# Kernel tuning notes

Hardware: AMD Instinct MI355X
Metric: run time of the kernel (lower is better)

Reference implementation:

```python
import jax, jax.numpy as jnp
import numpy as np

B, D, N, OUT, H = 32768, 256, 4, 512, 4
DH = D // H


def _layer_norm(x, g, b, eps=1e-5):
    mu = jnp.mean(x, axis=-1, keepdims=True)
    var = jnp.mean(jnp.square(x - mu), axis=-1, keepdims=True)
    return (x - mu) * jax.lax.rsqrt(var + eps) * g + b


def setup_inputs() -> dict:
    key = jax.random.key(0)
    ks = jax.random.split(key, 32)
    s = lambda i, shape, scale=0.02: (jax.random.normal(ks[i], shape, jnp.float32) * scale)
    inp = {
        'w0': jax.random.normal(ks[0], (B, D), jnp.float32),
        'w1': jax.random.normal(ks[1], (B, D), jnp.float32),
        'w2': jax.random.normal(ks[2], (B, D), jnp.float32),
        'w3': jax.random.normal(ks[3], (B, D), jnp.float32),
        'regime': jax.random.uniform(ks[4], (B, 4), jnp.float32),
        'tf_weights': jnp.array([0.5, 1.0, 1.5, 2.0], jnp.float32),
        'in_proj_w': s(5, (3 * D, D)),
        'in_proj_b': s(6, (3 * D,)),
        'out_proj_w': s(7, (D, D)),
        'out_proj_b': s(8, (D,)),
        'ln1_g': jnp.ones((D,), jnp.float32),
        'ln1_b': jnp.zeros((D,), jnp.float32),
        'sg_w': s(9, (D, 4)),
        'sg_b': s(10, (D,)),
        'sb_w': s(11, (D, 4)),
        'sb_b': s(12, (D,)),
        'f1_w': s(13, (2 * OUT, D * N)),
        'f1_b': s(14, (2 * OUT,)),
        'f2_w': s(15, (OUT, 2 * OUT)),
        'f2_b': s(16, (OUT,)),
        'ln2_g': jnp.ones((OUT,), jnp.float32),
        'ln2_b': jnp.zeros((OUT,), jnp.float32),
        'a1_w': s(17, (128, D * N)),
        'a1_b': s(18, (128,)),
        'a2_w': s(19, (1, 128)),
        'a2_b': s(20, (1,)),
    }
    return inp


def _forward(w0, w1, w2, w3, regime, tf_weights, in_proj_w, in_proj_b,
             out_proj_w, out_proj_b, ln1_g, ln1_b, sg_w, sg_b, sb_w, sb_b,
             f1_w, f1_b, f2_w, f2_b, ln2_g, ln2_b, a1_w, a1_b, a2_w, a2_b):
    weights = jax.nn.softmax(tf_weights)  # [N]
    wav = jnp.stack([w0, w1, w2, w3], axis=1)  # [B, N, D]
    weighted = wav * weights[None, :, None]    # [B, N, D]
    query = weighted[:, 0, :]                  # [B, D]

    # MultiheadAttention: q_len=1, kv_len=N, H heads
    wq, wk, wv = in_proj_w[:D], in_proj_w[D:2 * D], in_proj_w[2 * D:]
    bq, bk, bv = in_proj_b[:D], in_proj_b[D:2 * D], in_proj_b[2 * D:]
    q = (query @ wq.T + bq).reshape(B, H, DH)              # [B, H, Dh]
    k = (weighted @ wk.T + bk).reshape(B, N, H, DH)        # [B, N, H, Dh]
    v = (weighted @ wv.T + bv).reshape(B, N, H, DH)
    scores = jnp.einsum('bhd,bnhd->bhn', q, k) / jnp.sqrt(jnp.float32(DH))
    attn = jax.nn.softmax(scores, axis=-1)                 # [B, H, N]
    ctx = jnp.einsum('bhn,bnhd->bhd', attn, v).reshape(B, D)
    attn_out = ctx @ out_proj_w.T + out_proj_b             # [B, D]

    entry = _layer_norm(query + attn_out, ln1_g, ln1_b)    # [B, D]
    gamma = regime @ sg_w.T + sg_b
    beta = regime @ sb_w.T + sb_b
    entry = entry * (1.0 + gamma) + beta                   # FiLM

    cat = jnp.concatenate([entry, weighted[:, 1, :], weighted[:, 2, :], weighted[:, 3, :]], axis=-1)  # [B, D*N]
    h = jax.nn.gelu(cat @ f1_w.T + f1_b, approximate=False)
    fused = _layer_norm(h @ f2_w.T + f2_b, ln2_g, ln2_b)   # [B, OUT]

    a = jax.nn.gelu(cat @ a1_w.T + a1_b, approximate=False)
    alignment = jax.nn.sigmoid(a @ a2_w.T + a2_b)          # [B, 1]
    return fused, alignment


def reference(w0, w1, w2, w3, regime, tf_weights, in_proj_w, in_proj_b,
              out_proj_w, out_proj_b, ln1_g, ln1_b, sg_w, sg_b, sb_w, sb_b,
              f1_w, f1_b, f2_w, f2_b, ln2_g, ln2_b, a1_w, a1_b, a2_w, a2_b):
    return _forward(w0, w1, w2, w3, regime, tf_weights, in_proj_w, in_proj_b,
                    out_proj_w, out_proj_b, ln1_g, ln1_b, sg_w, sg_b, sb_w, sb_b,
                    f1_w, f1_b, f2_w, f2_b, ln2_g, ln2_b, a1_w, a1_b, a2_w, a2_b)
```

## Files before the change

kernel.cpp:

```cpp
#include <hip/hip_runtime.h>
#include <math.h>

#define NB 32768

typedef unsigned short u16;
typedef __attribute__((ext_vector_type(4))) float f32x4;
typedef __attribute__((ext_vector_type(8))) short bf16x8;

__device__ __forceinline__ float bf2f(u16 u){ return __uint_as_float(((unsigned int)u)<<16); }
__device__ __forceinline__ u16 f2bf(float f){
    unsigned int x = __float_as_uint(f);
    x += 0x7fffu + ((x>>16)&1u);
    return (u16)(x>>16);
}
__device__ __forceinline__ float gelu_f(float x){
    float z = fabsf(x) * 0.70710678118654752f;
    float t = __builtin_amdgcn_rcpf(1.0f + 0.3275911f*z);
    float p = t*(0.254829592f + t*(-0.284496736f + t*(1.421413741f + t*(-1.453152027f + t*1.061405429f))));
    float e = __expf(-z*z);
    float erf_abs = 1.0f - p*e;
    float erfv = copysignf(erf_abs, x);
    return 0.5f*x*(1.0f + erfv);
}

__device__ __forceinline__ void gload16(const void* g, void* l){
    __builtin_amdgcn_global_load_lds(
        (const __attribute__((address_space(1))) unsigned int*)g,
        (__attribute__((address_space(3))) unsigned int*)l, 16, 0, 0);
}

__global__ __launch_bounds__(256) void prepconv_kernel(
    const float* __restrict__ w0, const float* __restrict__ w1,
    const float* __restrict__ w2, const float* __restrict__ w3,
    const float* __restrict__ tfw, u16* __restrict__ wcat,
    const float* __restrict__ ipw_s, u16* __restrict__ ipw_d,
    const float* __restrict__ op_s,  u16* __restrict__ op_d,
    const float* __restrict__ f1_s,  u16* __restrict__ f1_d,
    const float* __restrict__ f2_s,  u16* __restrict__ f2_d,
    const float* __restrict__ a1_s,  u16* __restrict__ a1_d)
{
    const int blk = blockIdx.x, tid = threadIdx.x;
    if (blk < 8192){
        float t0=tfw[0], t1=tfw[1], t2=tfw[2], t3=tfw[3];
        float m = fmaxf(fmaxf(t0,t1), fmaxf(t2,t3));
        float e0=expf(t0-m), e1=expf(t1-m), e2=expf(t2-m), e3=expf(t3-m);
        float inv = 1.0f/(e0+e1+e2+e3);
        float s0=e0*inv, s1=e1*inv, s2=e2*inv, s3=e3*inv;

        int idx = blk*256 + tid;
        int b  = idx >> 6;
        int d4 = (idx & 63) << 2;
        size_t src = (size_t)b*256 + d4;
        float4 a0 = *reinterpret_cast<const float4*>(w0 + src);
        float4 a1 = *reinterpret_cast<const float4*>(w1 + src);
        float4 a2 = *reinterpret_cast<const float4*>(w2 + src);
        float4 a3 = *reinterpret_cast<const float4*>(w3 + src);
        size_t dst = (size_t)b*1024 + d4;
        ushort4 o;
        o.x=f2bf(a0.x*s0); o.y=f2bf(a0.y*s0); o.z=f2bf(a0.z*s0); o.w=f2bf(a0.w*s0);
        *reinterpret_cast<ushort4*>(wcat + dst) = o;
        o.x=f2bf(a1.x*s1); o.y=f2bf(a1.y*s1); o.z=f2bf(a1.z*s1); o.w=f2bf(a1.w*s1);
        *reinterpret_cast<ushort4*>(wcat + dst + 256) = o;
        o.x=f2bf(a2.x*s2); o.y=f2bf(a2.y*s2); o.z=f2bf(a2.z*s2); o.w=f2bf(a2.w*s2);
        *reinterpret_cast<ushort4*>(wcat + dst + 512) = o;
        o.x=f2bf(a3.x*s3); o.y=f2bf(a3.y*s3); o.z=f2bf(a3.z*s3); o.w=f2bf(a3.w*s3);
        *reinterpret_cast<ushort4*>(wcat + dst + 768) = o;
    } else {
        int i = (blk - 8192)*256 + tid;
        const float* s; u16* d; int off;
        if      (i < 49152)  { s=ipw_s; d=ipw_d; off=i; }
        else if (i < 65536)  { s=op_s;  d=op_d;  off=i-49152; }
        else if (i < 327680) { s=f1_s;  d=f1_d;  off=i-65536; }
        else if (i < 458752) { s=f2_s;  d=f2_d;  off=i-327680; }
        else                 { s=a1_s;  d=a1_d;  off=i-458752; }
        float4 v = reinterpret_cast<const float4*>(s)[off];
        ushort4 o; o.x=f2bf(v.x); o.y=f2bf(v.y); o.z=f2bf(v.z); o.w=f2bf(v.w);
        reinterpret_cast<ushort4*>(d)[off] = o;
    }
}

template<int ACT>
__global__ __launch_bounds__(256) void mgemm_kernel(
    const u16* __restrict__ A, int lda,
    const u16* __restrict__ W, int ldw,
    const float* __restrict__ bias,
    u16* __restrict__ C, int ldc, int K,
    const float* __restrict__ a2w, const float* __restrict__ a2b, float* __restrict__ aln)
{
    __shared__ __align__(16) u16 sA[4096];
    __shared__ __align__(16) u16 sB[4096];

    const int tid  = threadIdx.x;
    const int lane = tid & 63;
    const int wid  = tid >> 6;
    const int wr   = wid >> 1, wc = wid & 1;
    const int row0 = blockIdx.x << 7, col0 = blockIdx.y << 7;

    const int e0 = tid << 3,          r0s = e0 >> 5, c0s = e0 & 31;
    const int e1 = (256 + tid) << 3,  r1s = e1 >> 5, c1s = e1 & 31;
    const u16* gA0 = A + (size_t)(row0 + r0s)*lda + c0s;
    const u16* gA1 = A + (size_t)(row0 + r1s)*lda + c1s;
    const u16* gB0 = W + (size_t)(col0 + r0s)*ldw + c0s;
    const u16* gB1 = W + (size_t)(col0 + r1s)*ldw + c1s;
    u16* lA0 = sA + (wid << 9);
    u16* lA1 = sA + 2048 + (wid << 9);
    u16* lB0 = sB + (wid << 9);
    u16* lB1 = sB + 2048 + (wid << 9);

    const int la  = lane & 15;
    const int lk  = (lane >> 4) << 3;
    const int hi4 = (lane >> 4) << 2;
    const u16* rA = sA + (((wr << 6) + la) << 5) + lk;
    const u16* rB = sB + (((wc << 6) + la) << 5) + lk;

    f32x4 acc[4][4];
    {
        f32x4 binit[4];
        #pragma unroll
        for (int n=0;n<4;n++){
            float4 b4 = *reinterpret_cast<const float4*>(bias + col0 + (wc<<6) + (n<<4) + hi4);
            binit[n] = (f32x4){b4.x, b4.y, b4.z, b4.w};
        }
        #pragma unroll
        for (int m=0;m<4;m++)
            #pragma unroll
            for (int n=0;n<4;n++) acc[m][n] = binit[n];
    }

    for (int k0 = 0; k0 < K; k0 += 32){
        gload16(gA0 + k0, lA0);
        gload16(gA1 + k0, lA1);
        gload16(gB0 + k0, lB0);
        gload16(gB1 + k0, lB1);
        __syncthreads();
        bf16x8 af[4], bf[4];
        #pragma unroll
        for (int m=0;m<4;m++) af[m] = *reinterpret_cast<const bf16x8*>(rA + (m << 9));
        #pragma unroll
        for (int n=0;n<4;n++) bf[n] = *reinterpret_cast<const bf16x8*>(rB + (n << 9));
        #pragma unroll
        for (int m=0;m<4;m++)
            #pragma unroll
            for (int n=0;n<4;n++)
                acc[m][n] = __builtin_amdgcn_mfma_f32_16x16x32_bf16(bf[n], af[m], acc[m][n], 0, 0, 0);
        __syncthreads();
    }

    if (ACT == 2){
        float w4[4][4];
        #pragma unroll
        for (int n=0;n<4;n++){
            float4 t4 = *reinterpret_cast<const float4*>(a2w + (wc<<6) + (n<<4) + hi4);
            w4[n][0]=t4.x; w4[n][1]=t4.y; w4[n][2]=t4.z; w4[n][3]=t4.w;
        }
        float* red = reinterpret_cast<float*>(sA);
        #pragma unroll
        for (int m=0;m<4;m++){
            float p = 0.f;
            #pragma unroll
            for (int n=0;n<4;n++){
                f32x4 v = acc[m][n];
                p += gelu_f(v[0])*w4[n][0] + gelu_f(v[1])*w4[n][1]
                   + gelu_f(v[2])*w4[n][2] + gelu_f(v[3])*w4[n][3];
            }
            red[(((wr<<6) + (m<<4) + la) << 3) + (wc<<2) + (lane>>4)] = p;
        }
        __syncthreads();
        if (tid < 128){
            float s = 0.f;
            #pragma unroll
            for (int k2=0;k2<8;k2++) s += red[(tid<<3)+k2];
            aln[row0 + tid] = 1.0f/(1.0f + __expf(-(s + a2b[0])));
        }
        return;
    }

    #pragma unroll
    for (int m=0;m<4;m++){
        const int grow = row0 + (wr << 6) + (m << 4) + la;
        u16* crow = C + (size_t)grow*ldc + col0 + (wc << 6) + hi4;
        #pragma unroll
        for (int n=0;n<4;n++){
            f32x4 v = acc[m][n];
            float x0=v[0], x1=v[1], x2=v[2], x3=v[3];
            if (ACT == 1){ x0=gelu_f(x0); x1=gelu_f(x1); x2=gelu_f(x2); x3=gelu_f(x3); }
            ushort4 o; o.x=f2bf(x0); o.y=f2bf(x1); o.z=f2bf(x2); o.w=f2bf(x3);
            *reinterpret_cast<ushort4*>(crow + (n << 4)) = o;
        }
    }
}

template<int ACT>
__global__ __launch_bounds__(512) void gemm256p_kernel(
    const u16* __restrict__ A, int lda,
    const u16* __restrict__ W, int ldw,
    const float* __restrict__ bias,
    u16* __restrict__ C, int ldc, int K)
{
    __shared__ __align__(16) u16 sT[65536];

    const int tid  = threadIdx.x;
    const int lane = tid & 63;
    const int wid  = tid >> 6;
    const int wr   = wid >> 2;
    const int wc   = wid & 3;
    const int row0 = blockIdx.x << 8, col0 = blockIdx.y << 8;

    const int la = lane & 15;
    const int hi = lane >> 4;

    f32x4 acc[8][4];
    {
        f32x4 binit[4];
        #pragma unroll
        for (int n=0;n<4;n++){
            float4 b4 = *reinterpret_cast<const float4*>(bias + col0 + (wc<<6) + (n<<4) + (hi<<2));
            binit[n] = (f32x4){b4.x, b4.y, b4.z, b4.w};
        }
        #pragma unroll
        for (int m=0;m<8;m++)
            #pragma unroll
            for (int n=0;n<4;n++) acc[m][n] = binit[n];
    }

    const int rs = (wid << 4) + (lane >> 3);
    const int cs = ((lane & 7) ^ ((lane >> 3) & 7)) << 3;
    const u16* gA0 = A + (size_t)(row0 + rs)*lda + cs;
    const u16* gA1 = gA0 + (size_t)128*lda;
    const u16* gB0 = W + (size_t)(col0 + rs)*ldw + cs;
    const u16* gB1 = gB0 + (size_t)128*ldw;
    const int ldsw = (wid << 4) * 64;

    const int cph0 = (hi ^ (la & 7)) << 3;
    const u16* rAbase = sT + ((wr << 7) + la)*64;
    const u16* rBbase = sT + 16384 + ((wc << 6) + la)*64;

    const int NT = K >> 6;

    gload16(gB0, sT + 16384 + ldsw);          gload16(gB0 + 8*(size_t)ldw, sT + 16384 + ldsw + 512);
    gload16(gB1, sT + 24576 + ldsw);          gload16(gB1 + 8*(size_t)ldw, sT + 24576 + ldsw + 512);
    gload16(gA0, sT + ldsw);                  gload16(gA0 + 8*(size_t)lda, sT + ldsw + 512);
    gload16(gA1, sT + 8192 + ldsw);           gload16(gA1 + 8*(size_t)lda, sT + 8192 + ldsw + 512);

#define STG(GP, LD, DOFF) \
        gload16(GP + kb, sT + bn + (DOFF) + ldsw); \
        gload16(GP + kb + 8*(size_t)(LD), sT + bn + (DOFF) + ldsw + 512);

#define DSR(MH, KS) { \
        const int co_ = cph0 ^ ((KS) << 5); \
        const u16* rA_ = rAbase + b + ((MH) << 12) + co_; \
        const u16* rB_ = rBbase + b + co_; \
        af[0] = *reinterpret_cast<const bf16x8*>(rA_); \
        af[1] = *reinterpret_cast<const bf16x8*>(rA_ + 1024); \
        af[2] = *reinterpret_cast<const bf16x8*>(rA_ + 2048); \
        af[3] = *reinterpret_cast<const bf16x8*>(rA_ + 3072); \
        bf[0] = *reinterpret_cast<const bf16x8*>(rB_); \
        bf[1] = *reinterpret_cast<const bf16x8*>(rB_ + 1024); \
        bf[2] = *reinterpret_cast<const bf16x8*>(rB_ + 2048); \
        bf[3] = *reinterpret_cast<const bf16x8*>(rB_ + 3072); }

#define MFMA16(MB) { \
        __builtin_amdgcn_s_setprio(1); \
        _Pragma("unroll") \
        for (int m=0;m<4;m++){ \
            _Pragma("unroll") \
            for (int n=0;n<4;n++) \
                acc[(MB)+m][n] = __builtin_amdgcn_mfma_f32_16x16x32_bf16(bf[n], af[m], acc[(MB)+m][n], 0,0,0); \
        } \
        __builtin_amdgcn_s_setprio(0); }

    for (int t = 0; t < NT; ++t){
        const int b  = (t & 1) << 15;
        const int bn = b ^ 32768;
        const bool stg = (t + 1 < NT);
        const int kb = (t + 1) << 6;
        bf16x8 af[4], bf[4];

        asm volatile("s_waitcnt vmcnt(0)" ::: "memory");
        __builtin_amdgcn_s_barrier();
        __builtin_amdgcn_sched_barrier(0);
        DSR(0,0)
        if (stg){ STG(gB0, ldw, 16384) }
        MFMA16(0)
        DSR(1,0)
        if (stg){ STG(gB1, ldw, 24576) }
        __builtin_amdgcn_sched_barrier(0);
        __builtin_amdgcn_s_barrier();
        __builtin_amdgcn_sched_barrier(0);
        MFMA16(4)
        DSR(0,1)
        if (stg){ STG(gA0, lda, 0) }
        __builtin_amdgcn_sched_barrier(0);
        __builtin_amdgcn_s_barrier();
        __builtin_amdgcn_sched_barrier(0);
        MFMA16(0)
        DSR(1,1)
        if (stg){ STG(gA1, lda, 8192) }
        __builtin_amdgcn_sched_barrier(0);
        __builtin_amdgcn_s_barrier();
        __builtin_amdgcn_sched_barrier(0);
        MFMA16(4)
    }
#undef STG
#undef DSR
#undef MFMA16

    #pragma unroll
    for (int m=0;m<8;m++){
        const int grow = row0 + (wr << 7) + (m << 4) + la;
        u16* crow = C + (size_t)grow*ldc + col0 + (wc << 6) + (hi << 2);
        #pragma unroll
        for (int n=0;n<4;n++){
            f32x4 v = acc[m][n];
            float x0=v[0], x1=v[1], x2=v[2], x3=v[3];
            if (ACT == 1){ x0=gelu_f(x0); x1=gelu_f(x1); x2=gelu_f(x2); x3=gelu_f(x3); }
            ushort4 o; o.x=f2bf(x0); o.y=f2bf(x1); o.z=f2bf(x2); o.w=f2bf(x3);
            *reinterpret_cast<ushort4*>(crow + (n << 4)) = o;
        }
    }
}

__global__ __launch_bounds__(256) void attn_kernel(
    const u16* __restrict__ q, const u16* __restrict__ kv,
    u16* __restrict__ ctx)
{
    __shared__ float sQ[256], sK[1024], sV[1024], sS[16], sA[16];
    const int b = blockIdx.x, t = threadIdx.x;
    sQ[t] = bf2f(q[(size_t)b*256 + t]);
    #pragma unroll
    for (int n=0;n<4;n++){
        sK[n*256+t] = bf2f(kv[(size_t)b*2048 + n*512 + t]);
        sV[n*256+t] = bf2f(kv[(size_t)b*2048 + n*512 + 256 + t]);
    }
    __syncthreads();
    if (t < 16){
        int h = t>>2, n = t&3;
        float s = 0.f;
        const int o = h*64;
        #pragma unroll
        for (int dh=0; dh<64; ++dh) s += sQ[o+dh]*sK[n*256+o+dh];
        sS[t] = s * 0.125f;
    }
    __syncthreads();
    if (t < 4){
        float a0=sS[t*4+0], a1=sS[t*4+1], a2=sS[t*4+2], a3=sS[t*4+3];
        float m = fmaxf(fmaxf(a0,a1), fmaxf(a2,a3));
        float e0=expf(a0-m), e1=expf(a1-m), e2=expf(a2-m), e3=expf(a3-m);
        float inv = 1.0f/(e0+e1+e2+e3);
        sA[t*4+0]=e0*inv; sA[t*4+1]=e1*inv; sA[t*4+2]=e2*inv; sA[t*4+3]=e3*inv;
    }
    __syncthreads();
    const int h = t>>6;
    float c = sA[h*4+0]*sV[t] + sA[h*4+1]*sV[256+t] + sA[h*4+2]*sV[512+t] + sA[h*4+3]*sV[768+t];
    ctx[(size_t)b*256 + t] = f2bf(c);
}

__global__ __launch_bounds__(256) void lnfilm_kernel(
    u16* __restrict__ wcat, const u16* __restrict__ ao, const float* __restrict__ regime,
    const float* __restrict__ sgw, const float* __restrict__ sgb,
    const float* __restrict__ sbw, const float* __restrict__ sbb,
    const float* __restrict__ g1, const float* __restrict__ b1)
{
    const int b = blockIdx.x, t = threadIdx.x;
    float x = bf2f(wcat[(size_t)b*1024 + t]) + bf2f(ao[(size_t)b*256 + t]);
    float s = x, q = x*x;
    #pragma unroll
    for (int o=32;o;o>>=1){ s += __shfl_xor(s,o); q += __shfl_xor(q,o); }
    __shared__ float rs[4], rq[4];
    if ((t&63)==0){ rs[t>>6]=s; rq[t>>6]=q; }
    __syncthreads();
    s = rs[0]+rs[1]+rs[2]+rs[3];
    q = rq[0]+rq[1]+rq[2]+rq[3];
    float mu  = s*(1.0f/256.0f);
    float var = q*(1.0f/256.0f) - mu*mu;
    float rstd = rsqrtf(var + 1e-5f);
    float r0=regime[b*4+0], r1=regime[b*4+1], r2=regime[b*4+2], r3=regime[b*4+3];
    float gam = r0*sgw[t*4+0]+r1*sgw[t*4+1]+r2*sgw[t*4+2]+r3*sgw[t*4+3]+sgb[t];
    float bet = r0*sbw[t*4+0]+r1*sbw[t*4+1]+r2*sbw[t*4+2]+r3*sbw[t*4+3]+sbb[t];
    float e = ((x-mu)*rstd*g1[t]+b1[t])*(1.0f+gam)+bet;
    wcat[(size_t)b*1024 + t] = f2bf(e);
}

__global__ __launch_bounds__(256) void ln2_kernel(
    const u16* __restrict__ t1, const float* __restrict__ g, const float* __restrict__ bt,
    float* __restrict__ out)
{
    const int b = blockIdx.x, t = threadIdx.x;
    float x0 = bf2f(t1[(size_t)b*512 + t]);
    float x1 = bf2f(t1[(size_t)b*512 + 256 + t]);
    float s = x0+x1, q = x0*x0 + x1*x1;
    #pragma unroll
    for (int o=32;o;o>>=1){ s += __shfl_xor(s,o); q += __shfl_xor(q,o); }
    __shared__ float rs[4], rq[4];
    if ((t&63)==0){ rs[t>>6]=s; rq[t>>6]=q; }
    __syncthreads();
    s = rs[0]+rs[1]+rs[2]+rs[3];
    q = rq[0]+rq[1]+rq[2]+rq[3];
    float mu  = s*(1.0f/512.0f);
    float var = q*(1.0f/512.0f) - mu*mu;
    float rstd = rsqrtf(var + 1e-5f);
    out[(size_t)b*512 + t]       = (x0-mu)*rstd*g[t]     + bt[t];
    out[(size_t)b*512 + 256 + t] = (x1-mu)*rstd*g[256+t] + bt[256+t];
}

extern "C" void kernel_launch(void* const* d_in, const int* in_sizes, int n_in,
                              void* d_out, int out_size, void* d_ws, size_t ws_size,
                              hipStream_t stream) {
    const float* w0   = (const float*)d_in[0];
    const float* w1   = (const float*)d_in[1];
    const float* w2   = (const float*)d_in[2];
    const float* w3   = (const float*)d_in[3];
    const float* regime = (const float*)d_in[4];
    const float* tfw  = (const float*)d_in[5];
    const float* in_proj_w = (const float*)d_in[6];
    const float* in_proj_b = (const float*)d_in[7];
    const float* out_proj_w = (const float*)d_in[8];
    const float* out_proj_b = (const float*)d_in[9];
    const float* ln1_g = (const float*)d_in[10];
    const float* ln1_b = (const float*)d_in[11];
    const float* sg_w = (const float*)d_in[12];
    const float* sg_b = (const float*)d_in[13];
    const float* sb_w = (const float*)d_in[14];
    const float* sb_b = (const float*)d_in[15];
    const float* f1_w = (const float*)d_in[16];
    const float* f1_b = (const float*)d_in[17];
    const float* f2_w = (const float*)d_in[18];
    const float* f2_b = (const float*)d_in[19];
    const float* ln2_g = (const float*)d_in[20];
    const float* ln2_b = (const float*)d_in[21];
    const float* a1_w = (const float*)d_in[22];
    const float* a1_b = (const float*)d_in[23];
    const float* a2_w = (const float*)d_in[24];
    const float* a2_b = (const float*)d_in[25];

    char* ws = (char*)d_ws;
    u16* wcat  = (u16*)(ws);
    u16* qbuf  = (u16*)(ws + 67108864ull);
    u16* kvbuf = (u16*)(ws + 83886080ull);
    u16* hbuf  = kvbuf;
    u16* t1buf = (u16*)(ws + 150994944ull);
    u16* aobuf = (u16*)(ws + 184549376ull);
    u16* wb    = (u16*)(ws + 218103808ull);
    u16* ipw = wb;
    u16* opw = wb + 196608;
    u16* f1w = wb + 262144;
    u16* f2w = wb + 1310720;
    u16* a1w = wb + 1835008;

    float* out_fused = (float*)d_out;
    float* out_align = (float*)d_out + (size_t)NB*512;

    prepconv_kernel<<<10112, 256, 0, stream>>>(w0,w1,w2,w3,tfw,wcat,
        in_proj_w,ipw, out_proj_w,opw, f1_w,f1w, f2_w,f2w, a1_w,a1w);
    mgemm_kernel<0><<<dim3(256, 2), 256, 0, stream>>>(wcat, 1024, ipw, 256, in_proj_b, qbuf, 256, 256, nullptr, nullptr, nullptr);
    gemm256p_kernel<0><<<dim3(512, 2), 512, 0, stream>>>(wcat, 256, ipw+65536, 256, in_proj_b+256, kvbuf, 512, 256);
    attn_kernel<<<NB, 256, 0, stream>>>(qbuf, kvbuf, qbuf);
    mgemm_kernel<0><<<dim3(256, 2), 256, 0, stream>>>(qbuf, 256, opw, 256, out_proj_b, aobuf, 256, 256, nullptr, nullptr, nullptr);
    lnfilm_kernel<<<NB, 256, 0, stream>>>(wcat, aobuf, regime, sg_w, sg_b, sb_w, sb_b, ln1_g, ln1_b);
    gemm256p_kernel<1><<<dim3(128, 4), 512, 0, stream>>>(wcat, 1024, f1w, 1024, f1_b, hbuf, 1024, 1024);
    gemm256p_kernel<0><<<dim3(128, 2), 512, 0, stream>>>(hbuf, 1024, f2w, 1024, f2_b, t1buf, 512, 1024);
    ln2_kernel<<<NB, 256, 0, stream>>>(t1buf, ln2_g, ln2_b, out_fused);
    mgemm_kernel<2><<<dim3(256, 1), 256, 0, stream>>>(wcat, 1024, a1w, 1024, a1_b, qbuf, 128, 1024, a2_w, a2_b, out_align);
}
```

Before: 357.0 us.

## Shrink GEMM K-tile to 32 with single-barrier double-buffered pipeline

```diff
diff --git a/kernel.cpp b/kernel.cpp
--- a/kernel.cpp
+++ b/kernel.cpp
@@ -191,13 +191,13 @@
 }
 
 template<int ACT>
-__global__ __launch_bounds__(512) void gemm256p_kernel(
+__global__ __launch_bounds__(512) void gemm256b_kernel(
     const u16* __restrict__ A, int lda,
     const u16* __restrict__ W, int ldw,
     const float* __restrict__ bias,
     u16* __restrict__ C, int ldc, int K)
 {
-    __shared__ __align__(16) u16 sT[65536];
+    __shared__ __align__(16) u16 sT[32768];
 
     const int tid  = threadIdx.x;
     const int lane = tid & 63;
@@ -208,13 +208,14 @@
 
     const int la = lane & 15;
     const int hi = lane >> 4;
+    const int hi4 = hi << 2;
 
     f32x4 acc[8][4];
     {
         f32x4 binit[4];
         #pragma unroll
         for (int n=0;n<4;n++){
-            float4 b4 = *reinterpret_cast<const float4*>(bias + col0 + (wc<<6) + (n<<4) + (hi<<2));
+            float4 b4 = *reinterpret_cast<const float4*>(bias + col0 + (wc<<6) + (n<<4) + hi4);
             binit[n] = (f32x4){b4.x, b4.y, b4.z, b4.w};
         }
         #pragma unroll
@@ -223,92 +224,93 @@
             for (int n=0;n<4;n++) acc[m][n] = binit[n];
     }
 
-    const int rs = (wid << 4) + (lane >> 3);
-    const int cs = ((lane & 7) ^ ((lane >> 3) & 7)) << 3;
-    const u16* gA0 = A + (size_t)(row0 + rs)*lda + cs;
-    const u16* gA1 = gA0 + (size_t)128*lda;
-    const u16* gB0 = W + (size_t)(col0 + rs)*ldw + cs;
-    const u16* gB1 = gB0 + (size_t)128*ldw;
-    const int ldsw = (wid << 4) * 64;
-
-    const int cph0 = (hi ^ (la & 7)) << 3;
-    const u16* rAbase = sT + ((wr << 7) + la)*64;
-    const u16* rBbase = sT + 16384 + ((wc << 6) + la)*64;
-
-    const int NT = K >> 6;
-
-    gload16(gB0, sT + 16384 + ldsw);          gload16(gB0 + 8*(size_t)ldw, sT + 16384 + ldsw + 512);
-    gload16(gB1, sT + 24576 + ldsw);          gload16(gB1 + 8*(size_t)ldw, sT + 24576 + ldsw + 512);
-    gload16(gA0, sT + ldsw);                  gload16(gA0 + 8*(size_t)lda, sT + ldsw + 512);
-    gload16(gA1, sT + 8192 + ldsw);           gload16(gA1 + 8*(size_t)lda, sT + 8192 + ldsw + 512);
-
-#define STG(GP, LD, DOFF) \
-        gload16(GP + kb, sT + bn + (DOFF) + ldsw); \
-        gload16(GP + kb + 8*(size_t)(LD), sT + bn + (DOFF) + ldsw + 512);
-
-#define DSR(MH, KS) { \
-        const int co_ = cph0 ^ ((KS) << 5); \
-        const u16* rA_ = rAbase + b + ((MH) << 12) + co_; \
-        const u16* rB_ = rBbase + b + co_; \
-        af[0] = *reinterpret_cast<const bf16x8*>(rA_); \
-        af[1] = *reinterpret_cast<const bf16x8*>(rA_ + 1024); \
-        af[2] = *reinterpret_cast<const bf16x8*>(rA_ + 2048); \
-        af[3] = *reinterpret_cast<const bf16x8*>(rA_ + 3072); \
-        bf[0] = *reinterpret_cast<const bf16x8*>(rB_); \
-        bf[1] = *reinterpret_cast<const bf16x8*>(rB_ + 1024); \
-        bf[2] = *reinterpret_cast<const bf16x8*>(rB_ + 2048); \
-        bf[3] = *reinterpret_cast<const bf16x8*>(rB_ + 3072); }
-
-#define MFMA16(MB) { \
-        __builtin_amdgcn_s_setprio(1); \
-        _Pragma("unroll") \
-        for (int m=0;m<4;m++){ \
-            _Pragma("unroll") \
-            for (int n=0;n<4;n++) \
-                acc[(MB)+m][n] = __builtin_amdgcn_mfma_f32_16x16x32_bf16(bf[n], af[m], acc[(MB)+m][n], 0,0,0); \
-        } \
-        __builtin_amdgcn_s_setprio(0); }
+    const int rA0 = (wid << 5) + (lane >> 2);
+    const int rA1 = rA0 + 16;
+    const int sw0 = ((lane & 3) ^ ((rA0 >> 1) & 3)) << 3;
+    const int sw1 = ((lane & 3) ^ ((rA1 >> 1) & 3)) << 3;
+    const u16* pA0 = A + (size_t)(row0 + rA0)*lda + sw0;
+    const u16* pA1 = A + (size_t)(row0 + rA1)*lda + sw1;
+    const u16* pB0 = W + (size_t)(col0 + rA0)*ldw + sw0;
+    const u16* pB1 = W + (size_t)(col0 + rA1)*ldw + sw1;
+    const int ldsw = wid << 10;
+
+    const int cph0 = (hi ^ ((la >> 1) & 3)) << 3;
+    const u16* rAbase = sT + (((wr << 7) + la) << 5) + cph0;
+    const u16* rBbase = sT + 8192 + (((wc << 6) + la) << 5) + cph0;
+
+    const int NT = K >> 5;
+
+    gload16(pB0, sT + 8192 + ldsw);   gload16(pB1, sT + 8192 + ldsw + 512);
+    gload16(pA0, sT + ldsw);          gload16(pA1, sT + ldsw + 512);
 
     for (int t = 0; t < NT; ++t){
-        const int b  = (t & 1) << 15;
-        const int bn = b ^ 32768;
-        const bool stg = (t + 1 < NT);
-        const int kb = (t + 1) << 6;
-        bf16x8 af[4], bf[4];
+        const int b  = (t & 1) << 14;
+        const int bn = b ^ 16384;
+        const int kb = (t + 1) << 5;
 
         asm volatile("s_waitcnt vmcnt(0)" ::: "memory");
         __builtin_amdgcn_s_barrier();
-        __builtin_amdgcn_sched_barrier(0);
-        DSR(0,0)
-        if (stg){ STG(gB0, ldw, 16384) }
-        MFMA16(0)
-        DSR(1,0)
-        if (stg){ STG(gB1, ldw, 24576) }
-        __builtin_amdgcn_sched_barrier(0);
-        __builtin_amdgcn_s_barrier();
-        __builtin_amdgcn_sched_barrier(0);
-        MFMA16(4)
-        DSR(0,1)
-        if (stg){ STG(gA0, lda, 0) }
-        __builtin_amdgcn_sched_barrier(0);
-        __builtin_amdgcn_s_barrier();
-        __builtin_amdgcn_sched_barrier(0);
-        MFMA16(0)
-        DSR(1,1)
-        if (stg){ STG(gA1, lda, 8192) }
-        __builtin_amdgcn_sched_barrier(0);
-        __builtin_amdgcn_s_barrier();
-        __builtin_amdgcn_sched_barrier(0);
-        MFMA16(4)
-    }
-#undef STG
-#undef DSR
-#undef MFMA16
+
+        if (t + 1 < NT){
+            gload16(pB0 + kb, sT + bn + 8192 + ldsw);   gload16(pB1 + kb, sT + bn + 8192 + ldsw + 512);
+            gload16(pA0 + kb, sT + bn + ldsw);          gload16(pA1 + kb, sT + bn + ldsw + 512);
+        }
+
+        const u16* rA = rAbase + b;
+        const u16* rB = rBbase + b;
+        bf16x8 af0 = *reinterpret_cast<const bf16x8*>(rA);
+        bf16x8 af1 = *reinterpret_cast<const bf16x8*>(rA + 512);
+        bf16x8 af2 = *reinterpret_cast<const bf16x8*>(rA + 1024);
+        bf16x8 af3 = *reinterpret_cast<const bf16x8*>(rA + 1536);
+        bf16x8 bf0 = *reinterpret_cast<const bf16x8*>(rB);
+        bf16x8 bf1 = *reinterpret_cast<const bf16x8*>(rB + 512);
+        bf16x8 bf2 = *reinterpret_cast<const bf16x8*>(rB + 1024);
+        bf16x8 bf3 = *reinterpret_cast<const bf16x8*>(rB + 1536);
+        bf16x8 af4 = *reinterpret_cast<const bf16x8*>(rA + 2048);
+        bf16x8 af5 = *reinterpret_cast<const bf16x8*>(rA + 2560);
+        bf16x8 af6 = *reinterpret_cast<const bf16x8*>(rA + 3072);
+        bf16x8 af7 = *reinterpret_cast<const bf16x8*>(rA + 3584);
+
+        __builtin_amdgcn_s_setprio(1);
+        acc[0][0] = __builtin_amdgcn_mfma_f32_16x16x32_bf16(bf0, af0, acc[0][0], 0,0,0);
+        acc[0][1] = __builtin_amdgcn_mfma_f32_16x16x32_bf16(bf1, af0, acc[0][1], 0,0,0);
+        acc[0][2] = __builtin_amdgcn_mfma_f32_16x16x32_bf16(bf2, af0, acc[0][2], 0,0,0);
+        acc[0][3] = __builtin_amdgcn_mfma_f32_16x16x32_bf16(bf3, af0, acc[0][3], 0,0,0);
+        acc[1][0] = __builtin_amdgcn_mfma_f32_16x16x32_bf16(bf0, af1, acc[1][0], 0,0,0);
+        acc[1][1] = __builtin_amdgcn_mfma_f32_16x16x32_bf16(bf1, af1, acc[1][1], 0,0,0);
+        acc[1][2] = __builtin_amdgcn_mfma_f32_16x16x32_bf16(bf2, af1, acc[1][2], 0,0,0);
+        acc[1][3] = __builtin_amdgcn_mfma_f32_16x16x32_bf16(bf3, af1, acc[1][3], 0,0,0);
+        acc[2][0] = __builtin_amdgcn_mfma_f32_16x16x32_bf16(bf0, af2, acc[2][0], 0,0,0);
+        acc[2][1] = __builtin_amdgcn_mfma_f32_16x16x32_bf16(bf1, af2, acc[2][1], 0,0,0);
+        acc[2][2] = __builtin_amdgcn_mfma_f32_16x16x32_bf16(bf2, af2, acc[2][2], 0,0,0);
+        acc[2][3] = __builtin_amdgcn_mfma_f32_16x16x32_bf16(bf3, af2, acc[2][3], 0,0,0);
+        acc[3][0] = __builtin_amdgcn_mfma_f32_16x16x32_bf16(bf0, af3, acc[3][0], 0,0,0);
+        acc[3][1] = __builtin_amdgcn_mfma_f32_16x16x32_bf16(bf1, af3, acc[3][1], 0,0,0);
+        acc[3][2] = __builtin_amdgcn_mfma_f32_16x16x32_bf16(bf2, af3, acc[3][2], 0,0,0);
+        acc[3][3] = __builtin_amdgcn_mfma_f32_16x16x32_bf16(bf3, af3, acc[3][3], 0,0,0);
+        acc[4][0] = __builtin_amdgcn_mfma_f32_16x16x32_bf16(bf0, af4, acc[4][0], 0,0,0);
+        acc[4][1] = __builtin_amdgcn_mfma_f32_16x16x32_bf16(bf1, af4, acc[4][1], 0,0,0);
+        acc[4][2] = __builtin_amdgcn_mfma_f32_16x16x32_bf16(bf2, af4, acc[4][2], 0,0,0);
+        acc[4][3] = __builtin_amdgcn_mfma_f32_16x16x32_bf16(bf3, af4, acc[4][3], 0,0,0);
+        acc[5][0] = __builtin_amdgcn_mfma_f32_16x16x32_bf16(bf0, af5, acc[5][0], 0,0,0);
+        acc[5][1] = __builtin_amdgcn_mfma_f32_16x16x32_bf16(bf1, af5, acc[5][1], 0,0,0);
+        acc[5][2] = __builtin_amdgcn_mfma_f32_16x16x32_bf16(bf2, af5, acc[5][2], 0,0,0);
+        acc[5][3] = __builtin_amdgcn_mfma_f32_16x16x32_bf16(bf3, af5, acc[5][3], 0,0,0);
+        acc[6][0] = __builtin_amdgcn_mfma_f32_16x16x32_bf16(bf0, af6, acc[6][0], 0,0,0);
+        acc[6][1] = __builtin_amdgcn_mfma_f32_16x16x32_bf16(bf1, af6, acc[6][1], 0,0,0);
+        acc[6][2] = __builtin_amdgcn_mfma_f32_16x16x32_bf16(bf2, af6, acc[6][2], 0,0,0);
+        acc[6][3] = __builtin_amdgcn_mfma_f32_16x16x32_bf16(bf3, af6, acc[6][3], 0,0,0);
+        acc[7][0] = __builtin_amdgcn_mfma_f32_16x16x32_bf16(bf0, af7, acc[7][0], 0,0,0);
+        acc[7][1] = __builtin_amdgcn_mfma_f32_16x16x32_bf16(bf1, af7, acc[7][1], 0,0,0);
+        acc[7][2] = __builtin_amdgcn_mfma_f32_16x16x32_bf16(bf2, af7, acc[7][2], 0,0,0);
+        acc[7][3] = __builtin_amdgcn_mfma_f32_16x16x32_bf16(bf3, af7, acc[7][3], 0,0,0);
+        __builtin_amdgcn_s_setprio(0);
+    }
 
     #pragma unroll
     for (int m=0;m<8;m++){
         const int grow = row0 + (wr << 7) + (m << 4) + la;
-        u16* crow = C + (size_t)grow*ldc + col0 + (wc << 6) + (hi << 2);
+        u16* crow = C + (size_t)grow*ldc + col0 + (wc << 6) + hi4;
         #pragma unroll
         for (int n=0;n<4;n++){
             f32x4 v = acc[m][n];
@@ -453,12 +455,12 @@
     prepconv_kernel<<<10112, 256, 0, stream>>>(w0,w1,w2,w3,tfw,wcat,
         in_proj_w,ipw, out_proj_w,opw, f1_w,f1w, f2_w,f2w, a1_w,a1w);
     mgemm_kernel<0><<<dim3(256, 2), 256, 0, stream>>>(wcat, 1024, ipw, 256, in_proj_b, qbuf, 256, 256, nullptr, nullptr, nullptr);
-    gemm256p_kernel<0><<<dim3(512, 2), 512, 0, stream>>>(wcat, 256, ipw+65536, 256, in_proj_b+256, kvbuf, 512, 256);
+    gemm256b_kernel<0><<<dim3(512, 2), 512, 0, stream>>>(wcat, 256, ipw+65536, 256, in_proj_b+256, kvbuf, 512, 256);
     attn_kernel<<<NB, 256, 0, stream>>>(qbuf, kvbuf, qbuf);
     mgemm_kernel<0><<<dim3(256, 2), 256, 0, stream>>>(qbuf, 256, opw, 256, out_proj_b, aobuf, 256, 256, nullptr, nullptr, nullptr);
     lnfilm_kernel<<<NB, 256, 0, stream>>>(wcat, aobuf, regime, sg_w, sg_b, sb_w, sb_b, ln1_g, ln1_b);
-    gemm256p_kernel<1><<<dim3(128, 4), 512, 0, stream>>>(wcat, 1024, f1w, 1024, f1_b, hbuf, 1024, 1024);
-    gemm256p_kernel<0><<<dim3(128, 2), 512, 0, stream>>>(hbuf, 1024, f2w, 1024, f2_b, t1buf, 512, 1024);
+    gemm256b_kernel<1><<<dim3(128, 4), 512, 0, stream>>>(wcat, 1024, f1w, 1024, f1_b, hbuf, 1024, 1024);
+    gemm256b_kernel<0><<<dim3(128, 2), 512, 0, stream>>>(hbuf, 1024, f2w, 1024, f2_b, t1buf, 512, 1024);
     ln2_kernel<<<NB, 256, 0, stream>>>(t1buf, ln2_g, ln2_b, out_fused);
     mgemm_kernel<2><<<dim3(256, 1), 256, 0, stream>>>(wcat, 1024, a1w, 1024, a1_b, qbuf, 128, 1024, a2_w, a2_b, out_align);
 }
```

Result: slower. 368.5 us (+3.2%).

## Switch 256x256 GEMM to 32x32x16 MFMA and simplify staging schedule

Applied to the files above, without the earlier changes.

```diff
diff --git a/kernel.cpp b/kernel.cpp
--- a/kernel.cpp
+++ b/kernel.cpp
@@ -4,8 +4,9 @@
 #define NB 32768
 
 typedef unsigned short u16;
-typedef __attribute__((ext_vector_type(4))) float f32x4;
-typedef __attribute__((ext_vector_type(8))) short bf16x8;
+typedef __attribute__((ext_vector_type(4)))  float f32x4;
+typedef __attribute__((ext_vector_type(16))) float f32x16;
+typedef __attribute__((ext_vector_type(8)))  short bf16x8;
 
 __device__ __forceinline__ float bf2f(u16 u){ return __uint_as_float(((unsigned int)u)<<16); }
 __device__ __forceinline__ u16 f2bf(float f){
@@ -191,7 +192,7 @@
 }
 
 template<int ACT>
-__global__ __launch_bounds__(512) void gemm256p_kernel(
+__global__ __launch_bounds__(512) void gemm256c_kernel(
     const u16* __restrict__ A, int lda,
     const u16* __restrict__ W, int ldw,
     const float* __restrict__ bias,
@@ -206,21 +207,20 @@
     const int wc   = wid & 3;
     const int row0 = blockIdx.x << 8, col0 = blockIdx.y << 8;
 
-    const int la = lane & 15;
-    const int hi = lane >> 4;
-
-    f32x4 acc[8][4];
-    {
-        f32x4 binit[4];
-        #pragma unroll
-        for (int n=0;n<4;n++){
-            float4 b4 = *reinterpret_cast<const float4*>(bias + col0 + (wc<<6) + (n<<4) + (hi<<2));
-            binit[n] = (f32x4){b4.x, b4.y, b4.z, b4.w};
-        }
-        #pragma unroll
-        for (int m=0;m<8;m++)
-            #pragma unroll
-            for (int n=0;n<4;n++) acc[m][n] = binit[n];
+    const int l31 = lane & 31;
+    const int hi5 = lane >> 5;
+
+    f32x16 acc[4][2];
+    #pragma unroll
+    for (int nf=0; nf<2; nf++){
+        f32x16 bi;
+        #pragma unroll
+        for (int q=0; q<4; q++){
+            float4 b4 = *reinterpret_cast<const float4*>(bias + col0 + (wc<<6) + (nf<<5) + (q<<3) + (hi5<<2));
+            bi[4*q+0]=b4.x; bi[4*q+1]=b4.y; bi[4*q+2]=b4.z; bi[4*q+3]=b4.w;
+        }
+        #pragma unroll
+        for (int mf=0; mf<4; mf++) acc[mf][nf] = bi;
     }
 
     const int rs = (wid << 4) + (lane >> 3);
@@ -231,91 +231,69 @@
     const u16* gB1 = gB0 + (size_t)128*ldw;
     const int ldsw = (wid << 4) * 64;
 
-    const int cph0 = (hi ^ (la & 7)) << 3;
-    const u16* rAbase = sT + ((wr << 7) + la)*64;
-    const u16* rBbase = sT + 16384 + ((wc << 6) + la)*64;
+    const int arow = (wr << 7) + l31;
+    const int brow = (wc << 6) + l31;
 
     const int NT = K >> 6;
 
-    gload16(gB0, sT + 16384 + ldsw);          gload16(gB0 + 8*(size_t)ldw, sT + 16384 + ldsw + 512);
-    gload16(gB1, sT + 24576 + ldsw);          gload16(gB1 + 8*(size_t)ldw, sT + 24576 + ldsw + 512);
-    gload16(gA0, sT + ldsw);                  gload16(gA0 + 8*(size_t)lda, sT + ldsw + 512);
-    gload16(gA1, sT + 8192 + ldsw);           gload16(gA1 + 8*(size_t)lda, sT + 8192 + ldsw + 512);
-
-#define STG(GP, LD, DOFF) \
-        gload16(GP + kb, sT + bn + (DOFF) + ldsw); \
-        gload16(GP + kb + 8*(size_t)(LD), sT + bn + (DOFF) + ldsw + 512);
-
-#define DSR(MH, KS) { \
-        const int co_ = cph0 ^ ((KS) << 5); \
-        const u16* rA_ = rAbase + b + ((MH) << 12) + co_; \
-        const u16* rB_ = rBbase + b + co_; \
-        af[0] = *reinterpret_cast<const bf16x8*>(rA_); \
-        af[1] = *reinterpret_cast<const bf16x8*>(rA_ + 1024); \
-        af[2] = *reinterpret_cast<const bf16x8*>(rA_ + 2048); \
-        af[3] = *reinterpret_cast<const bf16x8*>(rA_ + 3072); \
-        bf[0] = *reinterpret_cast<const bf16x8*>(rB_); \
-        bf[1] = *reinterpret_cast<const bf16x8*>(rB_ + 1024); \
-        bf[2] = *reinterpret_cast<const bf16x8*>(rB_ + 2048); \
-        bf[3] = *reinterpret_cast<const bf16x8*>(rB_ + 3072); }
-
-#define MFMA16(MB) { \
-        __builtin_amdgcn_s_setprio(1); \
-        _Pragma("unroll") \
-        for (int m=0;m<4;m++){ \
-            _Pragma("unroll") \
-            for (int n=0;n<4;n++) \
-                acc[(MB)+m][n] = __builtin_amdgcn_mfma_f32_16x16x32_bf16(bf[n], af[m], acc[(MB)+m][n], 0,0,0); \
-        } \
-        __builtin_amdgcn_s_setprio(0); }
+    gload16(gB0, sT + 16384 + ldsw);  gload16(gB0 + 8*(size_t)ldw, sT + 16384 + ldsw + 512);
+    gload16(gB1, sT + 24576 + ldsw);  gload16(gB1 + 8*(size_t)ldw, sT + 24576 + ldsw + 512);
+    gload16(gA0, sT + ldsw);          gload16(gA0 + 8*(size_t)lda, sT + ldsw + 512);
+    gload16(gA1, sT + 8192 + ldsw);   gload16(gA1 + 8*(size_t)lda, sT + 8192 + ldsw + 512);
 
     for (int t = 0; t < NT; ++t){
         const int b  = (t & 1) << 15;
         const int bn = b ^ 32768;
-        const bool stg = (t + 1 < NT);
         const int kb = (t + 1) << 6;
-        bf16x8 af[4], bf[4];
 
         asm volatile("s_waitcnt vmcnt(0)" ::: "memory");
         __builtin_amdgcn_s_barrier();
         __builtin_amdgcn_sched_barrier(0);
-        DSR(0,0)
-        if (stg){ STG(gB0, ldw, 16384) }
-        MFMA16(0)
-        DSR(1,0)
-        if (stg){ STG(gB1, ldw, 24576) }
-        __builtin_amdgcn_sched_barrier(0);
-        __builtin_amdgcn_s_barrier();
-        __builtin_amdgcn_sched_barrier(0);
-        MFMA16(4)
-        DSR(0,1)
-        if (stg){ STG(gA0, lda, 0) }
-        __builtin_amdgcn_sched_barrier(0);
-        __builtin_amdgcn_s_barrier();
-        __builtin_amdgcn_sched_barrier(0);
-        MFMA16(0)
-        DSR(1,1)
-        if (stg){ STG(gA1, lda, 8192) }
-        __builtin_amdgcn_sched_barrier(0);
-        __builtin_amdgcn_s_barrier();
-        __builtin_amdgcn_sched_barrier(0);
-        MFMA16(4)
-    }
-#undef STG
-#undef DSR
-#undef MFMA16
-
-    #pragma unroll
-    for (int m=0;m<8;m++){
-        const int grow = row0 + (wr << 7) + (m << 4) + la;
-        u16* crow = C + (size_t)grow*ldc + col0 + (wc << 6) + (hi << 2);
-        #pragma unroll
-        for (int n=0;n<4;n++){
-            f32x4 v = acc[m][n];
-            float x0=v[0], x1=v[1], x2=v[2], x3=v[3];
-            if (ACT == 1){ x0=gelu_f(x0); x1=gelu_f(x1); x2=gelu_f(x2); x3=gelu_f(x3); }
-            ushort4 o; o.x=f2bf(x0); o.y=f2bf(x1); o.z=f2bf(x2); o.w=f2bf(x3);
-            *reinterpret_cast<ushort4*>(crow + (n << 4)) = o;
+
+        if (t + 1 < NT){
+            gload16(gB0 + kb, sT + bn + 16384 + ldsw);  gload16(gB0 + kb + 8*(size_t)ldw, sT + bn + 16384 + ldsw + 512);
+            gload16(gB1 + kb, sT + bn + 24576 + ldsw);  gload16(gB1 + kb + 8*(size_t)ldw, sT + bn + 24576 + ldsw + 512);
+            gload16(gA0 + kb, sT + bn + ldsw);          gload16(gA0 + kb + 8*(size_t)lda, sT + bn + ldsw + 512);
+            gload16(gA1 + kb, sT + bn + 8192 + ldsw);   gload16(gA1 + kb + 8*(size_t)lda, sT + bn + 8192 + ldsw + 512);
+        }
+
+        #pragma unroll
+        for (int ks=0; ks<4; ks++){
+            const int lc = (ks<<1) + hi5;
+            bf16x8 wf[2], af[4];
+            #pragma unroll
+            for (int nf=0; nf<2; nf++){
+                const int r = brow + (nf<<5);
+                wf[nf] = *reinterpret_cast<const bf16x8*>(sT + b + 16384 + r*64 + ((lc ^ (r&7))<<3));
+            }
+            #pragma unroll
+            for (int mf=0; mf<4; mf++){
+                const int r = arow + (mf<<5);
+                af[mf] = *reinterpret_cast<const bf16x8*>(sT + b + r*64 + ((lc ^ (r&7))<<3));
+            }
+            __builtin_amdgcn_s_setprio(1);
+            #pragma unroll
+            for (int mf=0; mf<4; mf++)
+                #pragma unroll
+                for (int nf=0; nf<2; nf++)
+                    acc[mf][nf] = __builtin_amdgcn_mfma_f32_32x32x16_bf16(wf[nf], af[mf], acc[mf][nf], 0, 0, 0);
+            __builtin_amdgcn_s_setprio(0);
+        }
+    }
+
+    #pragma unroll
+    for (int mf=0; mf<4; mf++){
+        const int grow = row0 + (wr<<7) + (mf<<5) + l31;
+        u16* crow = C + (size_t)grow*ldc + col0 + (wc<<6) + (hi5<<2);
+        #pragma unroll
+        for (int nf=0; nf<2; nf++){
+            #pragma unroll
+            for (int q=0; q<4; q++){
+                float x0=acc[mf][nf][4*q+0], x1=acc[mf][nf][4*q+1], x2=acc[mf][nf][4*q+2], x3=acc[mf][nf][4*q+3];
+                if (ACT==1){ x0=gelu_f(x0); x1=gelu_f(x1); x2=gelu_f(x2); x3=gelu_f(x3); }
+                ushort4 o; o.x=f2bf(x0); o.y=f2bf(x1); o.z=f2bf(x2); o.w=f2bf(x3);
+                *reinterpret_cast<ushort4*>(crow + (nf<<5) + (q<<3)) = o;
+            }
         }
     }
 }
@@ -453,12 +431,12 @@
     prepconv_kernel<<<10112, 256, 0, stream>>>(w0,w1,w2,w3,tfw,wcat,
         in_proj_w,ipw, out_proj_w,opw, f1_w,f1w, f2_w,f2w, a1_w,a1w);
     mgemm_kernel<0><<<dim3(256, 2), 256, 0, stream>>>(wcat, 1024, ipw, 256, in_proj_b, qbuf, 256, 256, nullptr, nullptr, nullptr);
-    gemm256p_kernel<0><<<dim3(512, 2), 512, 0, stream>>>(wcat, 256, ipw+65536, 256, in_proj_b+256, kvbuf, 512, 256);
+    gemm256c_kernel<0><<<dim3(512, 2), 512, 0, stream>>>(wcat, 256, ipw+65536, 256, in_proj_b+256, kvbuf, 512, 256);
     attn_kernel<<<NB, 256, 0, stream>>>(qbuf, kvbuf, qbuf);
     mgemm_kernel<0><<<dim3(256, 2), 256, 0, stream>>>(qbuf, 256, opw, 256, out_proj_b, aobuf, 256, 256, nullptr, nullptr, nullptr);
     lnfilm_kernel<<<NB, 256, 0, stream>>>(wcat, aobuf, regime, sg_w, sg_b, sb_w, sb_b, ln1_g, ln1_b);
-    gemm256p_kernel<1><<<dim3(128, 4), 512, 0, stream>>>(wcat, 1024, f1w, 1024, f1_b, hbuf, 1024, 1024);
-    gemm256p_kernel<0><<<dim3(128, 2), 512, 0, stream>>>(hbuf, 1024, f2w, 1024, f2_b, t1buf, 512, 1024);
+    gemm256c_kernel<1><<<dim3(128, 4), 512, 0, stream>>>(wcat, 1024, f1w, 1024, f1_b, hbuf, 1024, 1024);
+    gemm256c_kernel<0><<<dim3(128, 2), 512, 0, stream>>>(hbuf, 1024, f2w, 1024, f2_b, t1buf, 512, 1024);
     ln2_kernel<<<NB, 256, 0, stream>>>(t1buf, ln2_g, ln2_b, out_fused);
     mgemm_kernel<2><<<dim3(256, 1), 256, 0, stream>>>(wcat, 1024, a1w, 1024, a1_b, qbuf, 128, 1024, a2_w, a2_b, out_align);
 }
```

Measured after the change: 382.7 us. +7.2%, slower.
